# Kernel optimization log

Hardware: AMD Instinct MI355X
Metric: run time of the kernel (lower is better)

The kernel has to match this reference:

```python
import jax, jax.numpy as jnp
import numpy as np

D = 256       # dim
M = 50        # num_celltypes
NPATH = 65536 # path tokens (256*256)
N = M + NPATH
FF = 3        # focusing_factor
K = 5         # dwc kernel size


def find_closest_factors(num):
    for i in range(int(num ** 0.5), 0, -1):
        if num % i == 0:
            return (i, num // i)
    return (1, num)


def setup_inputs() -> dict:
    key = jax.random.key(0)
    ks = jax.random.split(key, 16)
    def w(k, shape, s=0.02):
        return jax.random.normal(k, shape, dtype=jnp.float32) * s
    z = lambda *s: jnp.zeros(s, jnp.float32)
    return {
        "x": jax.random.normal(ks[0], (1, N, D), dtype=jnp.float32),
        "W_qkv": w(ks[1], (D, 3 * D)),
        "scale_linear": w(ks[2], (1, 1, D)),
        "dwc_w": w(ks[3], (D, 1, K, K)),
        "dwc_b": w(ks[4], (D,)),
        "Wa": w(ks[5], (D, D)), "ba": z(D),
        "Wb": w(ks[6], (D, D)), "bb": z(D),
        "Wc": w(ks[7], (D, 1)), "bc": z(1),
        "W1": w(ks[8], (D, D)), "b1": z(D),
        "W2": w(ks[9], (D, D)), "b2": z(D),
        "W3a": w(ks[10], (2 * D, D)), "b3a": z(D),
        "W3b": w(ks[11], (D, D)), "b3b": z(D),
        "Wf": w(ks[12], (D, D)), "bf": z(D),
    }


def reference(x, W_qkv, scale_linear, dwc_w, dwc_b, Wa, ba, Wb, bb, Wc, bc,
              W1, b1, W2, b2, W3a, b3a, W3b, b3b, Wf, bf):
    scale = D ** -0.5
    qkv = x @ W_qkv                         # (1, N, 3D)
    q, k, v = jnp.split(qkv, 3, axis=-1)
    qc, qp = q[:, :M], q[:, M:]
    kc, kp = k[:, :M], k[:, M:]
    vc, vp = v[:, :M], v[:, M:]

    # --- softmax attention branches ---
    sa = jax.nn.softmax(jnp.einsum('bic,bjc->bij', qc * scale, kc), axis=-1)
    out_self_celltypes = sa @ vc            # (1, M, D)
    cap = jax.nn.softmax(jnp.einsum('bic,bjc->bij', qp * scale, kc), axis=-1)
    out_cross_path = cap @ vc               # (1, NPATH, D)
    cac = jax.nn.softmax(jnp.einsum('bic,bjc->bij', qc * scale, kp), axis=-1)
    out_cross_celltypes = cac @ vp          # (1, M, D)

    # --- focused linear attention on path tokens ---
    sp = jax.nn.softplus(scale_linear)
    ql = (jax.nn.relu(qp) + 1e-6) / sp
    kl = (jax.nn.relu(kp) + 1e-6) / sp
    qn = jnp.linalg.norm(ql, axis=-1, keepdims=True)
    kn = jnp.linalg.norm(kl, axis=-1, keepdims=True)
    ql = ql ** FF
    kl = kl ** FF
    ql = ql / jnp.linalg.norm(ql, axis=-1, keepdims=True) * qn
    kl = kl / jnp.linalg.norm(kl, axis=-1, keepdims=True) * kn
    zfac = 1.0 / (jnp.einsum('bic,bc->bi', ql, kl.sum(axis=1)) + 1e-6)
    kv = jnp.einsum('bjc,bjd->bcd', kl, vp)                 # (1, D, D)
    out_s = jnp.einsum('bic,bcd,bi->bid', ql, kv, zfac)     # (1, NPATH, D)

    # --- depthwise conv feature map ---
    wc, hc = find_closest_factors(NPATH)
    fm = vp.reshape(1, wc, hc, D).transpose(0, 3, 1, 2)     # b c w h
    fm = jax.lax.conv_general_dilated(
        fm, dwc_w, (1, 1), 'SAME',
        dimension_numbers=('NCHW', 'OIHW', 'NCHW'), feature_group_count=D)
    fm = fm + dwc_b[None, :, None, None]
    fm = fm.transpose(0, 2, 3, 1).reshape(1, NPATH, D)
    out_self_path = (out_s + fm) @ Wf + bf  # feamap_linear (dropout=eval)

    # --- gated attention net (shared weights, 4 calls) ---
    def gated(t):
        t = t[0]  # squeeze batch -> (n, D)
        a = jnp.tanh(t @ Wa + ba)
        g = jax.nn.sigmoid(t @ Wb + bb)
        return (a * g) @ Wc + bc  # (n, 1)

    A_cc = gated(out_cross_celltypes)
    A_cp = gated(out_cross_path)
    A_sc = gated(out_self_celltypes)
    A_sp = gated(out_self_path)

    # --- attention fusion (shared weights, 2 calls) ---
    def fuse(A1, A2, x1, x2):
        h1 = jax.nn.softmax(A1.T, axis=1) @ x1[0]   # (1, D)
        h1 = jax.nn.relu(h1 @ W1 + b1)
        h2 = jax.nn.softmax(A2.T, axis=1) @ x2[0]
        h2 = jax.nn.relu(h2 @ W2 + b2)
        f = jnp.concatenate([h1, h2], axis=1)       # (1, 2D)
        return jax.nn.relu(jax.nn.relu(f @ W3a + b3a) @ W3b + b3b)

    fusion_cross = fuse(A_cc, A_cp, out_cross_celltypes, out_cross_path)
    fusion_self = fuse(A_sc, A_sp, out_self_celltypes, out_self_path)
    return jnp.concatenate([fusion_cross, fusion_self], axis=1)  # (1, 2D)
```

## Files before the change

### kernel.cpp

```cpp
#include <hip/hip_runtime.h>
#include <hip/hip_bf16.h>
#include <math.h>


constexpr int DD = 256;
constexpr int MM = 50;
constexpr float SCL = 0.0625f;

constexpr size_t B_VPH = 0;
constexpr size_t B_QLH = (size_t)32 << 20;
constexpr size_t B_KLH = (size_t)64 << 20;
constexpr size_t B_E   = (size_t)96 << 20;
constexpr size_t B_SM  = (size_t)112 << 20;
constexpr size_t B_X   = B_SM + ((size_t)2 << 20);

constexpr size_t PP_OFF = (size_t)4 << 20;

constexpr size_t KLSUMR = 0;
constexpr size_t KLSUMP = 256;
constexpr size_t OCCDENP= 2304;
constexpr size_t W50P   = 2816;
constexpr size_t EDENP  = 3328;
constexpr size_t H2TP   = 3336;
constexpr size_t H2DENP = 5384;
constexpr size_t OCCRAW = 5392;
constexpr size_t ZEND   = 18192;
constexpr size_t QC     = ZEND;
constexpr size_t KC     = QC + 12800;
constexpr size_t VC     = KC + 12800;
constexpr size_t VCA    = VC + 12800;
constexpr size_t VCB    = VCA + 12800;
constexpr size_t WFA    = VCB + 12800;
constexpr size_t WFB    = WFA + 65536;
constexpr size_t BFA    = WFB + 65536;
constexpr size_t BFB    = BFA + 256;
constexpr size_t OSCB   = BFB + 256;
constexpr size_t OCCB   = OSCB + 12800;
constexpr size_t ASC    = OCCB + 12800;
constexpr size_t ACC50  = ASC + 64;
constexpr size_t SMEND  = ACC50 + 64;

constexpr size_t XT_WQKV = 0;
constexpr size_t XT_WFAT = 196608;
constexpr size_t XT_WFBT = 262144;
constexpr size_t XT_KVT  = 327680;
constexpr size_t XT_QCH  = 393216;
constexpr size_t XT_KCH  = 409600;
constexpr size_t XT_VCAT = 425984;
constexpr size_t XT_VCBT = 442368;
constexpr size_t XT_END  = 458752;
constexpr size_t WS_NEEDED = B_X + XT_END * 2;

typedef short bf16x8 __attribute__((ext_vector_type(8)));
typedef float f32x4 __attribute__((ext_vector_type(4)));

__device__ __forceinline__ float rcpf_(float x){ return __builtin_amdgcn_rcpf(x); }
__device__ __forceinline__ float fsig_(float x){ return rcpf_(1.0f + __expf(-x)); }
__device__ __forceinline__ float ftanh_(float x){ return 1.0f - 2.0f * rcpf_(__expf(2.0f * x) + 1.0f); }

__device__ __forceinline__ float bf2f(unsigned short u){
  return __uint_as_float(((unsigned int)u) << 16);
}
__device__ __forceinline__ unsigned short f2bf(float f){
  union { __hip_bfloat16 h; unsigned short u; } c;
  c.h = __float2bfloat16(f);
  return c.u;
}
__device__ __forceinline__ f32x4 mfma16(bf16x8 a, bf16x8 b, f32x4 c){
  return __builtin_amdgcn_mfma_f32_16x16x32_bf16(a, b, c, 0, 0, 0);
}

__device__ __forceinline__ float waveAllSum(float v){
  #pragma unroll
  for (int m = 1; m < 64; m <<= 1) v += __shfl_xor(v, m, 64);
  return v;
}

__device__ __forceinline__ size_t fragIdx(int n, int k, int K8){
  const int tile = n >> 4, cn = n & 15;
  const int k0 = k >> 5, kqi = (k >> 3) & 3, e = k & 7;
  return (((size_t)tile * K8 + k0) * 64 + (kqi * 16 + cn)) * 8 + e;
}

__device__ __forceinline__ int kvOff(int c, int k){
  return c * 40 + (c >> 3) * 8 + k;
}

__global__ void __launch_bounds__(256) k_prep0(const float* __restrict__ x, const float* __restrict__ Wqkv,
                                               float* qc, float* kc, float* vc,
                                               unsigned short* qch, unsigned short* kch,
                                               unsigned short* __restrict__ WT,
                                               const float* __restrict__ Wa, const float* __restrict__ Wb,
                                               const float* __restrict__ ba, const float* __restrict__ bb,
                                               const float* __restrict__ Wf, const float* __restrict__ bf,
                                               float* Wfa, float* Wfb, float* bfa, float* bfb,
                                               unsigned short* WfaTh, unsigned short* WfbTh){
  const int b = blockIdx.x, t = threadIdx.x;
  if (b < 48) {
    __shared__ unsigned short Tt[64][72];
    const int bn = b % 12, bk = b / 12;
    const int n0 = bn * 64, k0g = bk * 64;
    #pragma unroll
    for (int i = 0; i < 16; i++) {
      const int k_l = (t >> 6) + i * 4;
      const int n_l = t & 63;
      Tt[n_l][k_l] = f2bf(Wqkv[(size_t)(k0g + k_l) * 768 + n0 + n_l]);
    }
    __syncthreads();
    #pragma unroll
    for (int i = 0; i < 2; i++) {
      const int fr = t * 2 + i;
      const int t_l = fr >> 7;
      const int k0_l = (fr >> 6) & 1;
      const int lane_f = fr & 63;
      const int n_l = t_l * 16 + (lane_f & 15);
      const int k_l = k0_l * 32 + (lane_f >> 4) * 8;
      const int tg = (n0 >> 4) + t_l;
      const int k0gl = (k0g >> 5) + k0_l;
      bf16x8 v = *(const bf16x8*)&Tt[n_l][k_l];
      *(bf16x8*)&WT[(((size_t)tg * 8 + k0gl) * 64 + lane_f) * 8] = v;
    }
    return;
  }
  __shared__ float xs[256];
  const int j = t;
  if (b < 98) {
    const int r = b - 48;
    xs[j] = x[r * DD + j];
    __syncthreads();
    float aq = 0.f, ak = 0.f, av = 0.f;
    for (int k = 0; k < DD; k++) {
      float xv = xs[k];
      aq += xv * Wqkv[k * 768 + j];
      ak += xv * Wqkv[k * 768 + 256 + j];
      av += xv * Wqkv[k * 768 + 512 + j];
    }
    qc[r * DD + j] = aq; kc[r * DD + j] = ak; vc[r * DD + j] = av;
    qch[fragIdx(r, j, 8)] = f2bf(aq);
    kch[fragIdx(r, j, 8)] = f2bf(ak);
    if (r == 0) {
      for (int c = 50; c < 64; c++) {
        qch[fragIdx(c, j, 8)] = 0;
        kch[fragIdx(c, j, 8)] = 0;
      }
    }
    return;
  }
  const int bb2 = b - 98;
  const float* src; const float* Wm;
  if (bb2 < 256)      { src = Wf + bb2 * DD;         Wm = Wa; }
  else if (bb2 < 512) { src = Wf + (bb2 - 256) * DD; Wm = Wb; }
  else if (bb2 == 512){ src = bf;                    Wm = Wa; }
  else                { src = bf;                    Wm = Wb; }
  xs[j] = src[j];
  __syncthreads();
  float a = 0.f;
  for (int k = 0; k < DD; k++) a += xs[k] * Wm[k * DD + j];
  if (bb2 < 256)      { Wfa[bb2 * DD + j] = a; WfaTh[fragIdx(j, bb2, 8)] = f2bf(a); }
  else if (bb2 < 512) { Wfb[(bb2 - 256) * DD + j] = a; WfbTh[fragIdx(j, bb2 - 256, 8)] = f2bf(a); }
  else if (bb2 == 512) bfa[j] = a + ba[j];
  else bfb[j] = a + bb[j];
}

__global__ void __launch_bounds__(256) k_prep1g(const float* __restrict__ vc,
                                                const float* __restrict__ qc, const float* __restrict__ kc,
                                                const float* __restrict__ Wa, const float* __restrict__ Wb,
                                                const float* __restrict__ ba, const float* __restrict__ bb,
                                                const float* __restrict__ Wc, const float* __restrict__ bc,
                                                float* Vca, float* Vcb,
                                                unsigned short* VcaTh, unsigned short* VcbTh,
                                                float* __restrict__ osc, float* __restrict__ A){
  const int b = blockIdx.x, t = threadIdx.x;
  if (b < 50) {
    __shared__ float rs[256];
    const int r = b, j = t;
    rs[j] = vc[r * DD + j];
    __syncthreads();
    float a = 0.f, bv = 0.f;
    for (int k = 0; k < DD; k++) { float v = rs[k]; a += v * Wa[k * DD + j]; bv += v * Wb[k * DD + j]; }
    Vca[r * DD + j] = a; Vcb[r * DD + j] = bv;
    VcaTh[fragIdx(j, r, 2)] = f2bf(a);
    VcbTh[fragIdx(j, r, 2)] = f2bf(bv);
    if (r == 0) {
      for (int c = 50; c < 64; c++) {
        VcaTh[fragIdx(j, c, 2)] = 0;
        VcbTh[fragIdx(j, c, 2)] = 0;
      }
    }
    return;
  }
  const int i = b - 50;
  __shared__ float qs[256];
  __shared__ float P[64];
  __shared__ float red[4];
  qs[t] = qc[i * DD + t];
  __syncthreads();
  if (t < 64) {
    float s = -1e30f;
    if (t < 50) {
      float acc = 0.f;
      const float4* kr = (const float4*)&kc[t * DD];
      #pragma unroll 8
      for (int k = 0; k < 64; k++) {
        float4 kv = kr[k];
        float4 qv = *(const float4*)&qs[k * 4];
        acc += qv.x * kv.x + qv.y * kv.y + qv.z * kv.z + qv.w * kv.w;
      }
      s = acc * SCL;
    }
    float mx = s;
    #pragma unroll
    for (int m = 1; m < 64; m <<= 1) mx = fmaxf(mx, __shfl_xor(mx, m, 64));
    float e = (t < 50) ? __expf(s - mx) : 0.f;
    float den = waveAllSum(e);
    P[t] = e * rcpf_(den);
  }
  __syncthreads();
  float a = 0.f;
  for (int jj = 0; jj < 50; jj++) a += P[jj] * vc[jj * DD + t];
  osc[i * DD + t] = a;
  __syncthreads();
  qs[t] = a;
  __syncthreads();
  float u = 0.f, v = 0.f;
  for (int k = 0; k < DD; k++) { float tv = qs[k]; u += tv * Wa[k * DD + t]; v += tv * Wb[k * DD + t]; }
  float g = ftanh_(u + ba[t]) * fsig_(v + bb[t]) * Wc[t];
  g = waveAllSum(g);
  const int lane = t & 63, wv = t >> 6;
  if (lane == 0) red[wv] = g;
  __syncthreads();
  if (t == 0) A[i] = red[0] + red[1] + red[2] + red[3] + bc[0];
}

__global__ void __launch_bounds__(256) k_path1(
    const float* __restrict__ x, const unsigned short* __restrict__ WTf,
    const float* __restrict__ sln,
    const unsigned short* __restrict__ kchf, const unsigned short* __restrict__ qchf,
    const unsigned short* __restrict__ VcaTf, const unsigned short* __restrict__ VcbTf,
    const float* __restrict__ ba, const float* __restrict__ bb,
    const float* __restrict__ Wc, const float* __restrict__ bc,
    unsigned short* __restrict__ vph, unsigned short* __restrict__ qlh, unsigned short* __restrict__ klh,
    unsigned short* __restrict__ Eh, float* __restrict__ w50p, float* __restrict__ edenp, float* __restrict__ occdenp){
  __shared__ __align__(16) char arena[38912];
  unsigned short (*Psh)[72]   = (unsigned short (*)[72])arena;
  float (*denp)[4]            = (float (*)[4])(arena + 4608);
  unsigned short (*qpsb)[264] = (unsigned short (*)[264])(arena + 5120);
  unsigned short (*kpsb)[264] = (unsigned short (*)[264])(arena + 22016);

  const int tid = threadIdx.x;
  const int i0 = blockIdx.x * 32;
  const int part = blockIdx.x & 7;
  const int lane = tid & 63;
  const int wvv = tid >> 6;
  const int cn = lane & 15;
  const int m0 = (lane >> 4) * 4;
  const int kq = (lane >> 4) * 8;

  for (int l = tid; l < 2048; l += 256) {
    const int r = l >> 6, c4 = (l & 63) * 4;
    const float4 xv = *(const float4*)&x[(size_t)(MM + i0 + r) * DD + c4];
    ushort4 o; o.x = f2bf(xv.x); o.y = f2bf(xv.y); o.z = f2bf(xv.z); o.w = f2bf(xv.w);
    *(ushort4*)&qpsb[r][c4] = o;
  }
  __syncthreads();

  bf16x8 af0[8], af1[8];
  #pragma unroll
  for (int k0 = 0; k0 < 8; k0++) {
    af0[k0] = *(const bf16x8*)&qpsb[cn][k0 * 32 + kq];
    af1[k0] = *(const bf16x8*)&qpsb[16 + cn][k0 * 32 + kq];
  }
  __syncthreads();

  bf16x8 b0[8], b1[8];
  {
    const unsigned short* Bt = WTf + ((size_t)wvv * 8 * 64 + lane) * 8;
    #pragma unroll
    for (int k0 = 0; k0 < 8; k0++) b0[k0] = *(const bf16x8*)&Bt[(size_t)k0 * 512];
  }
  #pragma unroll 1
  for (int tt = 0; tt < 12; tt++) {
    const int t = wvv + 4 * tt;
    if (tt + 1 < 12) {
      const unsigned short* Bt = WTf + (((size_t)(t + 4) * 8) * 64 + lane) * 8;
      #pragma unroll
      for (int k0 = 0; k0 < 8; k0++) b1[k0] = *(const bf16x8*)&Bt[(size_t)k0 * 512];
    }
    f32x4 acc0 = {0.f, 0.f, 0.f, 0.f};
    f32x4 acc1 = {0.f, 0.f, 0.f, 0.f};
    #pragma unroll
    for (int k0 = 0; k0 < 8; k0++) {
      acc0 = mfma16(af0[k0], b0[k0], acc0);
      acc1 = mfma16(af1[k0], b0[k0], acc1);
    }
    if (t < 16) {
      int c = t * 16 + cn;
      #pragma unroll
      for (int i = 0; i < 4; i++) {
        qpsb[m0 + i][c] = f2bf(acc0[i]);
        qpsb[16 + m0 + i][c] = f2bf(acc1[i]);
      }
    } else if (t < 32) {
      int c = (t - 16) * 16 + cn;
      #pragma unroll
      for (int i = 0; i < 4; i++) {
        kpsb[m0 + i][c] = f2bf(acc0[i]);
        kpsb[16 + m0 + i][c] = f2bf(acc1[i]);
      }
    } else {
      int c = (t - 32) * 16 + cn;
      #pragma unroll
      for (int i = 0; i < 4; i++) {
        vph[(size_t)(i0 + m0 + i) * DD + c] = f2bf(acc0[i]);
        vph[(size_t)(i0 + 16 + m0 + i) * DD + c] = f2bf(acc1[i]);
      }
    }
    #pragma unroll
    for (int k0 = 0; k0 < 8; k0++) b0[k0] = b1[k0];
  }
  __syncthreads();

  float ep0[4], ep1[4];
  {
    f32x4 accp0 = {0.f,0.f,0.f,0.f}, accp1 = {0.f,0.f,0.f,0.f};
    f32x4 accc0 = {0.f,0.f,0.f,0.f}, accc1 = {0.f,0.f,0.f,0.f};
    const unsigned short* Bk = kchf + ((size_t)wvv * 8 * 64 + lane) * 8;
    const unsigned short* Bq = qchf + ((size_t)wvv * 8 * 64 + lane) * 8;
    #pragma unroll
    for (int k0 = 0; k0 < 8; k0++) {
      bf16x8 aq0 = *(const bf16x8*)&qpsb[cn][k0 * 32 + kq];
      bf16x8 aq1 = *(const bf16x8*)&qpsb[16 + cn][k0 * 32 + kq];
      bf16x8 ak0 = *(const bf16x8*)&kpsb[cn][k0 * 32 + kq];
      bf16x8 ak1 = *(const bf16x8*)&kpsb[16 + cn][k0 * 32 + kq];
      bf16x8 bk = *(const bf16x8*)&Bk[(size_t)k0 * 512];
      bf16x8 bq = *(const bf16x8*)&Bq[(size_t)k0 * 512];
      accp0 = mfma16(aq0, bk, accp0);
      accp1 = mfma16(aq1, bk, accp1);
      accc0 = mfma16(ak0, bq, accc0);
      accc1 = mfma16(ak1, bq, accc1);
    }
    const int col = wvv * 16 + cn;
    const bool ok = (col < 50);
    #pragma unroll
    for (int i = 0; i < 4; i++) {
      ep0[i] = ok ? __expf(accp0[i] * SCL) : 0.f;
      ep1[i] = ok ? __expf(accp1[i] * SCL) : 0.f;
    }
    float osum = 0.f;
    #pragma unroll
    for (int i = 0; i < 4; i++) {
      unsigned short h0 = ok ? f2bf(__expf(accc0[i] * SCL)) : (unsigned short)0;
      unsigned short h1 = ok ? f2bf(__expf(accc1[i] * SCL)) : (unsigned short)0;
      Eh[(size_t)(i0 + m0 + i) * 64 + col] = h0;
      Eh[(size_t)(i0 + 16 + m0 + i) * 64 + col] = h1;
      if (ok) osum += bf2f(h0) + bf2f(h1);
    }
    osum += __shfl_xor(osum, 16, 64);
    osum += __shfl_xor(osum, 32, 64);
    if (lane < 16 && ok) atomicAdd(&occdenp[part * 64 + col], osum);
    float d0[4], d1[4];
    #pragma unroll
    for (int i = 0; i < 4; i++) { d0[i] = ep0[i]; d1[i] = ep1[i]; }
    #pragma unroll
    for (int m = 1; m < 16; m <<= 1) {
      #pragma unroll
      for (int i = 0; i < 4; i++) {
        d0[i] += __shfl_xor(d0[i], m, 64);
        d1[i] += __shfl_xor(d1[i], m, 64);
      }
    }
    if (cn == 0) {
      #pragma unroll
      for (int i = 0; i < 4; i++) {
        denp[m0 + i][wvv] = d0[i];
        denp[16 + m0 + i][wvv] = d1[i];
      }
    }
  }
  __syncthreads();

  {
    const int col = wvv * 16 + cn;
    #pragma unroll
    for (int i = 0; i < 4; i++) {
      float4 dp = *(const float4*)&denp[m0 + i][0];
      Psh[m0 + i][col] = f2bf(ep0[i] * rcpf_(dp.x + dp.y + dp.z + dp.w));
      float4 dq = *(const float4*)&denp[16 + m0 + i][0];
      Psh[16 + m0 + i][col] = f2bf(ep1[i] * rcpf_(dq.x + dq.y + dq.z + dq.w));
    }
  }

  float4 sl4 = ((const float4*)sln)[lane];
  float4 rsp;
  rsp.x = rcpf_(log1pf(expf(sl4.x))); rsp.y = rcpf_(log1pf(expf(sl4.y)));
  rsp.z = rcpf_(log1pf(expf(sl4.z))); rsp.w = rcpf_(log1pf(expf(sl4.w)));
  float4 ba4 = ((const float4*)ba)[lane];
  float4 bb4 = ((const float4*)bb)[lane];
  float4 wc4 = ((const float4*)Wc)[lane];
  float bcv = bc[0];
  for (int rr = 0; rr < 8; rr++) {
    const int r = wvv * 8 + rr;
    const int row = i0 + r;
    ushort4 qu = *(const ushort4*)&qpsb[r][lane * 4];
    ushort4 ku = *(const ushort4*)&kpsb[r][lane * 4];
    float4 q4 = {bf2f(qu.x), bf2f(qu.y), bf2f(qu.z), bf2f(qu.w)};
    float4 k4 = {bf2f(ku.x), bf2f(ku.y), bf2f(ku.z), bf2f(ku.w)};
    float4 lq, lk;
    lq.x = (fmaxf(q4.x, 0.f) + 1e-6f) * rsp.x; lq.y = (fmaxf(q4.y, 0.f) + 1e-6f) * rsp.y;
    lq.z = (fmaxf(q4.z, 0.f) + 1e-6f) * rsp.z; lq.w = (fmaxf(q4.w, 0.f) + 1e-6f) * rsp.w;
    lk.x = (fmaxf(k4.x, 0.f) + 1e-6f) * rsp.x; lk.y = (fmaxf(k4.y, 0.f) + 1e-6f) * rsp.y;
    lk.z = (fmaxf(k4.z, 0.f) + 1e-6f) * rsp.z; lk.w = (fmaxf(k4.w, 0.f) + 1e-6f) * rsp.w;
    float4 q3, k3;
    q3.x = lq.x*lq.x*lq.x; q3.y = lq.y*lq.y*lq.y; q3.z = lq.z*lq.z*lq.z; q3.w = lq.w*lq.w*lq.w;
    k3.x = lk.x*lk.x*lk.x; k3.y = lk.y*lk.y*lk.y; k3.z = lk.z*lk.z*lk.z; k3.w = lk.w*lk.w*lk.w;
    float n1q = lq.x*lq.x + lq.y*lq.y + lq.z*lq.z + lq.w*lq.w;
    float n3q = q3.x*q3.x + q3.y*q3.y + q3.z*q3.z + q3.w*q3.w;
    float n1k = lk.x*lk.x + lk.y*lk.y + lk.z*lk.z + lk.w*lk.w;
    float n3k = k3.x*k3.x + k3.y*k3.y + k3.z*k3.z + k3.w*k3.w;
    n1q = waveAllSum(n1q); n3q = waveAllSum(n3q);
    n1k = waveAllSum(n1k); n3k = waveAllSum(n3k);
    float fq = sqrtf(n1q * rcpf_(n3q));
    float fk = sqrtf(n1k * rcpf_(n3k));
    ushort4 qo, ko;
    qo.x = f2bf(q3.x * fq); qo.y = f2bf(q3.y * fq); qo.z = f2bf(q3.z * fq); qo.w = f2bf(q3.w * fq);
    ko.x = f2bf(k3.x * fk); ko.y = f2bf(k3.y * fk); ko.z = f2bf(k3.z * fk); ko.w = f2bf(k3.w * fk);
    *(ushort4*)&qlh[(size_t)row * DD + lane * 4] = qo;
    *(ushort4*)&klh[(size_t)row * DD + lane * 4] = ko;
  }
  __syncthreads();

  {
    bf16x8 ap0[2], ap1[2];
    #pragma unroll
    for (int k0 = 0; k0 < 2; k0++) {
      ap0[k0] = *(const bf16x8*)&Psh[cn][k0 * 32 + kq];
      ap1[k0] = *(const bf16x8*)&Psh[16 + cn][k0 * 32 + kq];
    }
    #pragma unroll 1
    for (int tt = 0; tt < 4; tt++) {
      const int nt = wvv * 4 + tt;
      const unsigned short* Bu = VcaTf + (((size_t)nt * 2) * 64 + lane) * 8;
      const unsigned short* Bv = VcbTf + (((size_t)nt * 2) * 64 + lane) * 8;
      f32x4 au0 = {0.f,0.f,0.f,0.f}, au1 = {0.f,0.f,0.f,0.f};
      f32x4 av0 = {0.f,0.f,0.f,0.f}, av1 = {0.f,0.f,0.f,0.f};
      #pragma unroll
      for (int k0 = 0; k0 < 2; k0++) {
        bf16x8 bu = *(const bf16x8*)&Bu[(size_t)k0 * 512];
        bf16x8 bv = *(const bf16x8*)&Bv[(size_t)k0 * 512];
        au0 = mfma16(ap0[k0], bu, au0);
        au1 = mfma16(ap1[k0], bu, au1);
        av0 = mfma16(ap0[k0], bv, av0);
        av1 = mfma16(ap1[k0], bv, av1);
      }
      #pragma unroll
      for (int i = 0; i < 4; i++) {
        qpsb[m0 + i][nt * 16 + cn] = f2bf(au0[i]);
        qpsb[16 + m0 + i][nt * 16 + cn] = f2bf(au1[i]);
        kpsb[m0 + i][nt * 16 + cn] = f2bf(av0[i]);
        kpsb[16 + m0 + i][nt * 16 + cn] = f2bf(av1[i]);
      }
    }
  }
  __syncthreads();

  #pragma unroll
  for (int rr = 0; rr < 8; rr++) {
    const int r = wvv * 8 + rr;
    ushort4 uu = *(const ushort4*)&qpsb[r][lane * 4];
    ushort4 vv = *(const ushort4*)&kpsb[r][lane * 4];
    float g = ftanh_(bf2f(uu.x) + ba4.x) * fsig_(bf2f(vv.x) + bb4.x) * wc4.x
            + ftanh_(bf2f(uu.y) + ba4.y) * fsig_(bf2f(vv.y) + bb4.y) * wc4.y
            + ftanh_(bf2f(uu.z) + ba4.z) * fsig_(bf2f(vv.z) + bb4.z) * wc4.z
            + ftanh_(bf2f(uu.w) + ba4.w) * fsig_(bf2f(vv.w) + bb4.w) * wc4.w;
    g = waveAllSum(g);
    if (lane == 0) *(float*)&Psh[r][64] = __expf(g + bcv);
  }
  __syncthreads();
  if (tid < 64) {
    float s = 0.f;
    #pragma unroll
    for (int r = 0; r < 32; r++) s += *(const float*)&Psh[r][64] * bf2f(Psh[r][tid]);
    atomicAdd(&w50p[part * 64 + tid], s);
  }
  if (tid == 0) {
    float es = 0.f;
    #pragma unroll
    for (int r = 0; r < 32; r++) es += *(const float*)&Psh[r][64];
    atomicAdd(&edenp[part], es);
  }
}

__global__ void __launch_bounds__(256) k_kv(const unsigned short* __restrict__ klh,
                                            const unsigned short* __restrict__ Eh,
                                            const unsigned short* __restrict__ vph,
                                            unsigned short* __restrict__ PP,
                                            float* __restrict__ klsump,
                                            float* __restrict__ occraw){
  __shared__ __align__(16) unsigned short AT[2][2608];
  __shared__ __align__(16) unsigned short BvpT[2][10480];
  const int tid = threadIdx.x;
  const int lane = tid & 63;
  const int wvv = tid >> 6;
  const int cn = lane & 15;
  const int m0 = (lane >> 4) * 4;
  const int kq = (lane >> 4) * 8;
  const int cb = blockIdx.x;
  const int z  = blockIdx.y;
  const int jj = tid >> 3;
  const int c8 = (tid & 7) * 8;
  const bool isOcc = (cb == 4);

  f32x4 acc[4][4];
  f32x4 acc1[4];
  #pragma unroll
  for (int mt = 0; mt < 4; mt++) {
    acc1[mt] = (f32x4){0.f,0.f,0.f,0.f};
    #pragma unroll
    for (int tl = 0; tl < 4; tl++) acc[mt][tl] = (f32x4){0.f,0.f,0.f,0.f};
  }
  bf16x8 ones;
  #pragma unroll
  for (int i = 0; i < 8; i++) ones[i] = (short)0x3F80;

  const int jbase = z * 1024;
  {
    const int j0 = jbase;
    bf16x8 av;
    if (isOcc) av = *(const bf16x8*)&Eh[(size_t)(j0 + jj) * 64 + c8];
    else       av = *(const bf16x8*)&klh[(size_t)(j0 + jj) * 256 + cb * 64 + c8];
    #pragma unroll
    for (int i = 0; i < 8; i++) AT[0][kvOff(c8 + i, jj)] = (unsigned short)av[i];
    #pragma unroll
    for (int rep = 0; rep < 4; rep++) {
      bf16x8 bv = *(const bf16x8*)&vph[(size_t)(j0 + jj) * 256 + rep * 64 + c8];
      #pragma unroll
      for (int i = 0; i < 8; i++) BvpT[0][kvOff(rep * 64 + c8 + i, jj)] = (unsigned short)bv[i];
    }
  }
  __syncthreads();

  #pragma unroll 1
  for (int step = 0; step < 32; step++) {
    const int cur = step & 1;
    bf16x8 avn, bvn[4];
    if (step + 1 < 32) {
      const int j0 = jbase + (step + 1) * 32;
      if (isOcc) avn = *(const bf16x8*)&Eh[(size_t)(j0 + jj) * 64 + c8];
      else       avn = *(const bf16x8*)&klh[(size_t)(j0 + jj) * 256 + cb * 64 + c8];
      #pragma unroll
      for (int rep = 0; rep < 4; rep++)
        bvn[rep] = *(const bf16x8*)&vph[(size_t)(j0 + jj) * 256 + rep * 64 + c8];
    }
    bf16x8 afr[4], bfr[4];
    #pragma unroll
    for (int mt = 0; mt < 4; mt++)
      afr[mt] = *(const bf16x8*)&AT[cur][kvOff(cn + mt * 16, kq)];
    #pragma unroll
    for (int tl = 0; tl < 4; tl++)
      bfr[tl] = *(const bf16x8*)&BvpT[cur][kvOff(wvv * 64 + tl * 16 + cn, kq)];
    if (!isOcc) {
      #pragma unroll
      for (int mt = 0; mt < 4; mt++) acc1[mt] = mfma16(afr[mt], ones, acc1[mt]);
    }
    #pragma unroll
    for (int mt = 0; mt < 4; mt++)
      #pragma unroll
      for (int tl = 0; tl < 4; tl++) acc[mt][tl] = mfma16(afr[mt], bfr[tl], acc[mt][tl]);
    if (step + 1 < 32) {
      const int nb = cur ^ 1;
      #pragma unroll
      for (int i = 0; i < 8; i++) AT[nb][kvOff(c8 + i, jj)] = (unsigned short)avn[i];
      #pragma unroll
      for (int rep = 0; rep < 4; rep++)
        #pragma unroll
        for (int i = 0; i < 8; i++) BvpT[nb][kvOff(rep * 64 + c8 + i, jj)] = (unsigned short)bvn[rep][i];
    }
    __syncthreads();
  }
  if (isOcc) {
    #pragma unroll
    for (int mt = 0; mt < 4; mt++)
      #pragma unroll
      for (int i = 0; i < 4; i++) {
        const int ri = mt * 16 + m0 + i;
        if (ri < 50) {
          #pragma unroll
          for (int tl = 0; tl < 4; tl++) {
            const int d = wvv * 64 + tl * 16 + cn;
            atomicAdd(&occraw[ri * DD + d], acc[mt][tl][i]);
          }
        }
      }
    return;
  }
  unsigned short* P = PP + ((size_t)(cb * 64 + z)) * 16384;
  #pragma unroll
  for (int mt = 0; mt < 4; mt++)
    #pragma unroll
    for (int tl = 0; tl < 4; tl++) {
      const int n = (wvv * 4 + tl) * 16 + cn;
      #pragma unroll
      for (int i = 0; i < 4; i++)
        P[(size_t)(mt * 16 + m0 + i) * 256 + n] = f2bf(acc[mt][tl][i]);
    }
  if (wvv == 0 && cn == 0) {
    #pragma unroll
    for (int mt = 0; mt < 4; mt++)
      #pragma unroll
      for (int i = 0; i < 4; i++)
        atomicAdd(&klsump[(z & 7) * 256 + cb * 64 + mt * 16 + m0 + i], acc1[mt][i]);
  }
}

__global__ void __launch_bounds__(256) k_fin2(const unsigned short* __restrict__ PP,
                                              unsigned short* __restrict__ kvTf,
                                              const float* __restrict__ occraw,
                                              const float* __restrict__ occdenp,
                                              float* __restrict__ occ,
                                              const float* __restrict__ klsump,
                                              float* __restrict__ klsum,
                                              const float* __restrict__ Wa, const float* __restrict__ Wb,
                                              const float* __restrict__ ba, const float* __restrict__ bb,
                                              const float* __restrict__ Wc, const float* __restrict__ bc,
                                              float* __restrict__ A){
  __shared__ float ts[256];
  __shared__ float red[4];
  const int b = blockIdx.x, tid = threadIdx.x;
  if (b < 32) {
    const int gm = b * 8 + (tid >> 5);
    const int cb = gm >> 6, m = gm & 63;
    const int d8 = (tid & 31) * 8;
    float s[8];
    #pragma unroll
    for (int e = 0; e < 8; e++) s[e] = 0.f;
    for (int z = 0; z < 64; z++) {
      bf16x8 v = *(const bf16x8*)&PP[((size_t)(cb * 64 + z)) * 16384 + (size_t)m * 256 + d8];
      #pragma unroll
      for (int e = 0; e < 8; e++) s[e] += bf2f((unsigned short)v[e]);
    }
    #pragma unroll
    for (int e = 0; e < 8; e++)
      kvTf[fragIdx(d8 + e, gm, 8)] = f2bf(s[e]);
  } else if (b < 82) {
    const int i = b - 32, j = tid;
    float den = 0.f;
    #pragma unroll
    for (int p = 0; p < 8; p++) den += occdenp[p * 64 + i];
    float t = occraw[i * DD + j] / den;
    occ[i * DD + j] = t;
    ts[j] = t;
    __syncthreads();
    float u = 0.f, v = 0.f;
    for (int k = 0; k < DD; k++) { float tv = ts[k]; u += tv * Wa[k * DD + j]; v += tv * Wb[k * DD + j]; }
    float g = ftanh_(u + ba[j]) * fsig_(v + bb[j]) * Wc[j];
    g = waveAllSum(g);
    const int lane = j & 63, wv = j >> 6;
    if (lane == 0) red[wv] = g;
    __syncthreads();
    if (j == 0) A[i] = red[0] + red[1] + red[2] + red[3] + bc[0];
  } else {
    const int d = tid;
    float s = 0.f;
    #pragma unroll
    for (int p = 0; p < 8; p++) s += klsump[p * 256 + d];
    klsum[d] = s;
  }
}

__global__ void __launch_bounds__(256) k_tail(const unsigned short* __restrict__ qlh,
                                              const unsigned short* __restrict__ kvTf,
                                              const float* __restrict__ klsum,
                                              const unsigned short* __restrict__ vph,
                                              const float* __restrict__ dwcw, const float* __restrict__ dwcb,
                                              const unsigned short* __restrict__ WfaTf,
                                              const unsigned short* __restrict__ WfbTf,
                                              const float* __restrict__ bfa, const float* __restrict__ bfb,
                                              const float* __restrict__ Wc, const float* __restrict__ bc,
                                              float* __restrict__ h2tp, float* __restrict__ h2denp){
  __shared__ unsigned short Tsh[32][264];
  __shared__ unsigned short OSb[32][264];
  __shared__ unsigned short aVb[32][264];
  __shared__ float zf[32];
  __shared__ float ev[32];
  const int tid = threadIdx.x;
  const int i0 = blockIdx.x * 32;
  const int part = blockIdx.x & 7;
  const int lane = tid & 63;
  const int wvv = tid >> 6;
  const int cn = lane & 15;
  const int m0 = (lane >> 4) * 4;
  const int kq = (lane >> 4) * 8;
  for (int l = tid; l < 2048; l += 256) {
    int r = l >> 6, c4 = (l & 63) * 4;
    *(ushort4*)&Tsh[r][c4] = *(const ushort4*)&qlh[(size_t)(i0 + r) * DD + c4];
  }
  __syncthreads();
  {
    bf16x8 afq0[8], afq1[8];
    #pragma unroll
    for (int k0 = 0; k0 < 8; k0++) {
      afq0[k0] = *(const bf16x8*)&Tsh[cn][k0 * 32 + kq];
      afq1[k0] = *(const bf16x8*)&Tsh[16 + cn][k0 * 32 + kq];
    }
    #pragma unroll 1
    for (int tt = 0; tt < 4; tt++) {
      const int nt = wvv * 4 + tt;
      const unsigned short* Bt = kvTf + (((size_t)nt * 8) * 64 + lane) * 8;
      f32x4 acc0 = {0.f,0.f,0.f,0.f};
      f32x4 acc1 = {0.f,0.f,0.f,0.f};
      #pragma unroll
      for (int k0 = 0; k0 < 8; k0++) {
        bf16x8 b = *(const bf16x8*)&Bt[(size_t)k0 * 512];
        acc0 = mfma16(afq0[k0], b, acc0);
        acc1 = mfma16(afq1[k0], b, acc1);
      }
      #pragma unroll
      for (int i = 0; i < 4; i++) {
        OSb[m0 + i][nt * 16 + cn] = f2bf(acc0[i]);
        OSb[16 + m0 + i][nt * 16 + cn] = f2bf(acc1[i]);
      }
    }
  }
  {
    float4 ks4 = ((const float4*)klsum)[lane];
    #pragma unroll
    for (int rr = 0; rr < 8; rr++) {
      const int r = wvv * 8 + rr;
      ushort4 q4 = *(const ushort4*)&Tsh[r][lane * 4];
      float s = bf2f(q4.x)*ks4.x + bf2f(q4.y)*ks4.y + bf2f(q4.z)*ks4.z + bf2f(q4.w)*ks4.w;
      s = waveAllSum(s);
      if (lane == 0) zf[r] = rcpf_(s + 1e-6f);
    }
  }
  __syncthreads();
  const int j = tid;
  float w[25];
  #pragma unroll
  for (int t = 0; t < 25; t++) w[t] = dwcw[j * 25 + t];
  const float bias = dwcb[j];
  const int y = i0 >> 8, x0 = i0 & 255;
  float fm[32];
  #pragma unroll
  for (int r = 0; r < 32; r++) fm[r] = bias;
  #pragma unroll
  for (int dy = -2; dy <= 2; dy++) {
    const int yy = y + dy;
    if ((unsigned)yy > 255u) continue;
    float buf[36];
    #pragma unroll
    for (int i = 0; i < 36; i++) {
      const int xx = x0 - 2 + i;
      buf[i] = ((unsigned)xx <= 255u) ? bf2f(vph[(size_t)((yy << 8) + xx) * DD + j]) : 0.f;
    }
    const float* wr = &w[(dy + 2) * 5];
    #pragma unroll
    for (int r = 0; r < 32; r++)
      fm[r] += buf[r] * wr[0] + buf[r+1] * wr[1] + buf[r+2] * wr[2]
             + buf[r+3] * wr[3] + buf[r+4] * wr[4];
  }
  #pragma unroll
  for (int r = 0; r < 32; r++) {
    fm[r] = bf2f(OSb[r][j]) * zf[r] + fm[r];
    Tsh[r][j] = f2bf(fm[r]);
  }
  __syncthreads();
  {
    bf16x8 aft0[8], aft1[8];
    #pragma unroll
    for (int k0 = 0; k0 < 8; k0++) {
      aft0[k0] = *(const bf16x8*)&Tsh[cn][k0 * 32 + kq];
      aft1[k0] = *(const bf16x8*)&Tsh[16 + cn][k0 * 32 + kq];
    }
    #pragma unroll 1
    for (int jb = 0; jb < 8; jb++) {
      const int nt = wvv * 4 + (jb & 3);
      const unsigned short* Bt = ((jb < 4) ? WfaTf : WfbTf) + (((size_t)nt * 8) * 64 + lane) * 8;
      f32x4 acc0 = {0.f,0.f,0.f,0.f};
      f32x4 acc1 = {0.f,0.f,0.f,0.f};
      #pragma unroll
      for (int k0 = 0; k0 < 8; k0++) {
        bf16x8 b = *(const bf16x8*)&Bt[(size_t)k0 * 512];
        acc0 = mfma16(aft0[k0], b, acc0);
        acc1 = mfma16(aft1[k0], b, acc1);
      }
      unsigned short (*dst)[264] = (jb < 4) ? OSb : aVb;
      #pragma unroll
      for (int i = 0; i < 4; i++) {
        dst[m0 + i][nt * 16 + cn] = f2bf(acc0[i]);
        dst[16 + m0 + i][nt * 16 + cn] = f2bf(acc1[i]);
      }
    }
  }
  __syncthreads();
  {
    float4 bfa4 = ((const float4*)bfa)[lane];
    float4 bfb4 = ((const float4*)bfb)[lane];
    float4 wc4 = ((const float4*)Wc)[lane];
    const float bcv = bc[0];
    #pragma unroll
    for (int rr = 0; rr < 8; rr++) {
      const int r = wvv * 8 + rr;
      ushort4 uu = *(const ushort4*)&OSb[r][lane * 4];
      ushort4 vv = *(const ushort4*)&aVb[r][lane * 4];
      float g = ftanh_(bf2f(uu.x) + bfa4.x) * fsig_(bf2f(vv.x) + bfb4.x) * wc4.x
              + ftanh_(bf2f(uu.y) + bfa4.y) * fsig_(bf2f(vv.y) + bfb4.y) * wc4.y
              + ftanh_(bf2f(uu.z) + bfa4.z) * fsig_(bf2f(vv.z) + bfb4.z) * wc4.z
              + ftanh_(bf2f(uu.w) + bfa4.w) * fsig_(bf2f(vv.w) + bfb4.w) * wc4.w;
      g = waveAllSum(g);
      if (lane == 0) ev[r] = __expf(g + bcv);
    }
  }
  __syncthreads();
  float hp = 0.f;
  #pragma unroll
  for (int r = 0; r < 32; r++) hp += ev[r] * fm[r];
  atomicAdd(&h2tp[part * 256 + j], hp);
  if (tid == 0) {
    float es = 0.f;
    #pragma unroll
    for (int r = 0; r < 32; r++) es += ev[r];
    atomicAdd(&h2denp[part], es);
  }
}

__global__ void __launch_bounds__(256) k_final(
    const float* __restrict__ A_cc, const float* __restrict__ occ,
    const float* __restrict__ A_sc, const float* __restrict__ osc,
    const float* __restrict__ w50p, const float* __restrict__ edenp,
    const float* __restrict__ h2tp, const float* __restrict__ h2denp,
    const float* __restrict__ vc, const float* __restrict__ Wf, const float* __restrict__ bf,
    const float* __restrict__ W1, const float* __restrict__ b1,
    const float* __restrict__ W2, const float* __restrict__ b2,
    const float* __restrict__ W3a, const float* __restrict__ b3a,
    const float* __restrict__ W3b, const float* __restrict__ b3b,
    float* __restrict__ out){
  int j = threadIdx.x;
  __shared__ float pw[64];
  __shared__ float w50t[64];
  __shared__ float t1[256], t2[256], fz[512], z1[256];
  if (blockIdx.x == 0) {
    if (j < 64) {
      float s = 0.f;
      #pragma unroll
      for (int p = 0; p < 8; p++) s += w50p[p * 64 + j];
      w50t[j] = s;
    }
    float edentot = 0.f;
    #pragma unroll
    for (int p = 0; p < 8; p++) edentot += edenp[p];
    if (j < 64) pw[j] = (j < 50) ? expf(A_cc[j]) : 0.f;
    __syncthreads();
    float den = 0.f;
    for (int i = 0; i < 50; i++) den += pw[i];
    float raw = 0.f;
    for (int i = 0; i < 50; i++) raw += pw[i] * occ[i * DD + j];
    t1[j] = raw / den;
    float r2 = 0.f;
    for (int i = 0; i < 50; i++) r2 += w50t[i] * vc[i * DD + j];
    t2[j] = r2 / edentot;
    __syncthreads();
    float a1 = 0.f, a2 = 0.f;
    for (int k = 0; k < DD; k++) { a1 += t1[k] * W1[k * DD + j]; a2 += t2[k] * W2[k * DD + j]; }
    fz[j] = fmaxf(a1 + b1[j], 0.f);
    fz[256 + j] = fmaxf(a2 + b2[j], 0.f);
    __syncthreads();
    float z = 0.f;
    for (int k = 0; k < 512; k++) z += fz[k] * W3a[k * DD + j];
    z1[j] = fmaxf(z + b3a[j], 0.f);
    __syncthreads();
    float o = 0.f;
    for (int k = 0; k < DD; k++) o += z1[k] * W3b[k * DD + j];
    out[j] = fmaxf(o + b3b[j], 0.f);
  } else {
    float h2dentot = 0.f;
    #pragma unroll
    for (int p = 0; p < 8; p++) h2dentot += h2denp[p];
    if (j < 64) pw[j] = (j < 50) ? expf(A_sc[j]) : 0.f;
    {
      float s = 0.f;
      #pragma unroll
      for (int p = 0; p < 8; p++) s += h2tp[p * 256 + j];
      t2[j] = s / h2dentot;
    }
    __syncthreads();
    float den = 0.f;
    for (int i = 0; i < 50; i++) den += pw[i];
    float raw = 0.f;
    for (int i = 0; i < 50; i++) raw += pw[i] * osc[i * DD + j];
    t1[j] = raw / den;
    float hs = 0.f;
    for (int k = 0; k < DD; k++) hs += t2[k] * Wf[k * DD + j];
    __syncthreads();
    t2[j] = hs + bf[j];
    __syncthreads();
    float a1 = 0.f, a2 = 0.f;
    for (int k = 0; k < DD; k++) { a1 += t1[k] * W1[k * DD + j]; a2 += t2[k] * W2[k * DD + j]; }
    fz[j] = fmaxf(a1 + b1[j], 0.f);
    fz[256 + j] = fmaxf(a2 + b2[j], 0.f);
    __syncthreads();
    float z = 0.f;
    for (int k = 0; k < 512; k++) z += fz[k] * W3a[k * DD + j];
    z1[j] = fmaxf(z + b3a[j], 0.f);
    __syncthreads();
    float o = 0.f;
    for (int k = 0; k < DD; k++) o += z1[k] * W3b[k * DD + j];
    out[256 + j] = fmaxf(o + b3b[j], 0.f);
  }
}

extern "C" void kernel_launch(void* const* d_in, const int* in_sizes, int n_in,
                              void* d_out, int out_size, void* d_ws, size_t ws_size,
                              hipStream_t stream) {
  if (ws_size < WS_NEEDED) return;
  const float* x   = (const float*)d_in[0];
  const float* Wqkv= (const float*)d_in[1];
  const float* sln = (const float*)d_in[2];
  const float* dwcw= (const float*)d_in[3];
  const float* dwcb= (const float*)d_in[4];
  const float* Wa  = (const float*)d_in[5];
  const float* ba  = (const float*)d_in[6];
  const float* Wb  = (const float*)d_in[7];
  const float* bb  = (const float*)d_in[8];
  const float* Wc  = (const float*)d_in[9];
  const float* bc  = (const float*)d_in[10];
  const float* W1  = (const float*)d_in[11];
  const float* b1  = (const float*)d_in[12];
  const float* W2  = (const float*)d_in[13];
  const float* b2  = (const float*)d_in[14];
  const float* W3a = (const float*)d_in[15];
  const float* b3a = (const float*)d_in[16];
  const float* W3b = (const float*)d_in[17];
  const float* b3b = (const float*)d_in[18];
  const float* Wf  = (const float*)d_in[19];
  const float* bf  = (const float*)d_in[20];

  char* wsb = (char*)d_ws;
  unsigned short* VPH = (unsigned short*)(wsb + B_VPH);
  unsigned short* QLH = (unsigned short*)(wsb + B_QLH);
  unsigned short* KLH = (unsigned short*)(wsb + B_KLH);
  unsigned short* EHB = (unsigned short*)(wsb + B_E);
  unsigned short* PPB = EHB + PP_OFF;
  float* SM = (float*)(wsb + B_SM);
  unsigned short* XT = (unsigned short*)(wsb + B_X);
  float* outp = (float*)d_out;

  hipMemsetAsync((void*)SM, 0, ZEND * sizeof(float), stream);

  k_prep0<<<612, 256, 0, stream>>>(x, Wqkv, SM + QC, SM + KC, SM + VC,
                                   XT + XT_QCH, XT + XT_KCH, XT + XT_WQKV,
                                   Wa, Wb, ba, bb, Wf, bf,
                                   SM + WFA, SM + WFB, SM + BFA, SM + BFB,
                                   XT + XT_WFAT, XT + XT_WFBT);
  k_prep1g<<<100, 256, 0, stream>>>(SM + VC, SM + QC, SM + KC,
                                    Wa, Wb, ba, bb, Wc, bc,
                                    SM + VCA, SM + VCB, XT + XT_VCAT, XT + XT_VCBT,
                                    SM + OSCB, SM + ASC);

  k_path1<<<2048, 256, 0, stream>>>(x, XT + XT_WQKV, sln, XT + XT_KCH, XT + XT_QCH,
                                    XT + XT_VCAT, XT + XT_VCBT, ba, bb, Wc, bc,
                                    VPH, QLH, KLH, EHB, SM + W50P, SM + EDENP, SM + OCCDENP);
  k_kv<<<dim3(5, 64), 256, 0, stream>>>(KLH, EHB, VPH, PPB, SM + KLSUMP, SM + OCCRAW);
  k_fin2<<<83, 256, 0, stream>>>(PPB, XT + XT_KVT,
                                 SM + OCCRAW, SM + OCCDENP, SM + OCCB,
                                 SM + KLSUMP, SM + KLSUMR,
                                 Wa, Wb, ba, bb, Wc, bc, SM + ACC50);

  k_tail<<<2048, 256, 0, stream>>>(QLH, XT + XT_KVT, SM + KLSUMR, VPH, dwcw, dwcb,
                                   XT + XT_WFAT, XT + XT_WFBT, SM + BFA, SM + BFB,
                                   Wc, bc, SM + H2TP, SM + H2DENP);

  k_final<<<2, 256, 0, stream>>>(SM + ACC50, SM + OCCB, SM + ASC, SM + OSCB,
                                 SM + W50P, SM + EDENP, SM + H2TP, SM + H2DENP,
                                 SM + VC, Wf, bf, W1, b1, W2, b2, W3a, b3a, W3b, b3b, outp);
}
```

Measured before the change: 470.1 us.

## Accumulate KV partials via fp32 atomics and double token split in k_kv

k_kv now adds each block's KV partial into a single fp32 accumulator with atomicAdd instead of writing per-slice bf16 partial buffers. k_fin2 then only converts that accumulator to the fragment layout, with no 64-way reduction. The token range per block is halved and the grid doubled to 5x128 for more parallelism. This removes the partial-buffer write and read-back, but adds many contended global atomics and changes the summation order.

New measurement: 500.2 us. 6.4% more time.

```diff
diff --git a/kernel.cpp b/kernel.cpp
--- a/kernel.cpp
+++ b/kernel.cpp
@@ -13,8 +13,6 @@
 constexpr size_t B_E   = (size_t)96 << 20;
 constexpr size_t B_SM  = (size_t)112 << 20;
 constexpr size_t B_X   = B_SM + ((size_t)2 << 20);
-
-constexpr size_t PP_OFF = (size_t)4 << 20;
 
 constexpr size_t KLSUMR = 0;
 constexpr size_t KLSUMP = 256;
@@ -24,7 +22,8 @@
 constexpr size_t H2TP   = 3336;
 constexpr size_t H2DENP = 5384;
 constexpr size_t OCCRAW = 5392;
-constexpr size_t ZEND   = 18192;
+constexpr size_t KVACC  = 18192;
+constexpr size_t ZEND   = KVACC + 65536;
 constexpr size_t QC     = ZEND;
 constexpr size_t KC     = QC + 12800;
 constexpr size_t VC     = KC + 12800;
@@ -493,7 +492,7 @@
 __global__ void __launch_bounds__(256) k_kv(const unsigned short* __restrict__ klh,
                                             const unsigned short* __restrict__ Eh,
                                             const unsigned short* __restrict__ vph,
-                                            unsigned short* __restrict__ PP,
+                                            float* __restrict__ kvacc,
                                             float* __restrict__ klsump,
                                             float* __restrict__ occraw){
   __shared__ __align__(16) unsigned short AT[2][2608];
@@ -522,7 +521,7 @@
   #pragma unroll
   for (int i = 0; i < 8; i++) ones[i] = (short)0x3F80;
 
-  const int jbase = z * 1024;
+  const int jbase = z * 512;
   {
     const int j0 = jbase;
     bf16x8 av;
@@ -540,10 +539,10 @@
   __syncthreads();
 
   #pragma unroll 1
-  for (int step = 0; step < 32; step++) {
+  for (int step = 0; step < 16; step++) {
     const int cur = step & 1;
     bf16x8 avn, bvn[4];
-    if (step + 1 < 32) {
+    if (step + 1 < 16) {
       const int j0 = jbase + (step + 1) * 32;
       if (isOcc) avn = *(const bf16x8*)&Eh[(size_t)(j0 + jj) * 64 + c8];
       else       avn = *(const bf16x8*)&klh[(size_t)(j0 + jj) * 256 + cb * 64 + c8];
@@ -566,7 +565,7 @@
     for (int mt = 0; mt < 4; mt++)
       #pragma unroll
       for (int tl = 0; tl < 4; tl++) acc[mt][tl] = mfma16(afr[mt], bfr[tl], acc[mt][tl]);
-    if (step + 1 < 32) {
+    if (step + 1 < 16) {
       const int nb = cur ^ 1;
       #pragma unroll
       for (int i = 0; i < 8; i++) AT[nb][kvOff(c8 + i, jj)] = (unsigned short)avn[i];
@@ -593,7 +592,6 @@
       }
     return;
   }
-  unsigned short* P = PP + ((size_t)(cb * 64 + z)) * 16384;
   #pragma unroll
   for (int mt = 0; mt < 4; mt++)
     #pragma unroll
@@ -601,7 +599,7 @@
       const int n = (wvv * 4 + tl) * 16 + cn;
       #pragma unroll
       for (int i = 0; i < 4; i++)
-        P[(size_t)(mt * 16 + m0 + i) * 256 + n] = f2bf(acc[mt][tl][i]);
+        atomicAdd(&kvacc[(size_t)(cb * 64 + mt * 16 + m0 + i) * 256 + n], acc[mt][tl][i]);
     }
   if (wvv == 0 && cn == 0) {
     #pragma unroll
@@ -612,7 +610,7 @@
   }
 }
 
-__global__ void __launch_bounds__(256) k_fin2(const unsigned short* __restrict__ PP,
+__global__ void __launch_bounds__(256) k_fin2(const float* __restrict__ kvacc,
                                               unsigned short* __restrict__ kvTf,
                                               const float* __restrict__ occraw,
                                               const float* __restrict__ occdenp,
@@ -626,23 +624,19 @@
   __shared__ float ts[256];
   __shared__ float red[4];
   const int b = blockIdx.x, tid = threadIdx.x;
-  if (b < 32) {
-    const int gm = b * 8 + (tid >> 5);
-    const int cb = gm >> 6, m = gm & 63;
-    const int d8 = (tid & 31) * 8;
-    float s[8];
-    #pragma unroll
-    for (int e = 0; e < 8; e++) s[e] = 0.f;
-    for (int z = 0; z < 64; z++) {
-      bf16x8 v = *(const bf16x8*)&PP[((size_t)(cb * 64 + z)) * 16384 + (size_t)m * 256 + d8];
-      #pragma unroll
-      for (int e = 0; e < 8; e++) s[e] += bf2f((unsigned short)v[e]);
-    }
-    #pragma unroll
-    for (int e = 0; e < 8; e++)
-      kvTf[fragIdx(d8 + e, gm, 8)] = f2bf(s[e]);
-  } else if (b < 82) {
-    const int i = b - 32, j = tid;
+  if (b < 8) {
+    const int gm = b * 32 + (tid >> 3);
+    const int d0 = (tid & 7) * 32;
+    #pragma unroll 8
+    for (int q = 0; q < 8; q++) {
+      float4 v = *(const float4*)&kvacc[(size_t)gm * 256 + d0 + q * 4];
+      kvTf[fragIdx(d0 + q * 4 + 0, gm, 8)] = f2bf(v.x);
+      kvTf[fragIdx(d0 + q * 4 + 1, gm, 8)] = f2bf(v.y);
+      kvTf[fragIdx(d0 + q * 4 + 2, gm, 8)] = f2bf(v.z);
+      kvTf[fragIdx(d0 + q * 4 + 3, gm, 8)] = f2bf(v.w);
+    }
+  } else if (b < 58) {
+    const int i = b - 8, j = tid;
     float den = 0.f;
     #pragma unroll
     for (int p = 0; p < 8; p++) den += occdenp[p * 64 + i];
@@ -939,7 +933,6 @@
   unsigned short* QLH = (unsigned short*)(wsb + B_QLH);
   unsigned short* KLH = (unsigned short*)(wsb + B_KLH);
   unsigned short* EHB = (unsigned short*)(wsb + B_E);
-  unsigned short* PPB = EHB + PP_OFF;
   float* SM = (float*)(wsb + B_SM);
   unsigned short* XT = (unsigned short*)(wsb + B_X);
   float* outp = (float*)d_out;
@@ -959,8 +952,8 @@
   k_path1<<<2048, 256, 0, stream>>>(x, XT + XT_WQKV, sln, XT + XT_KCH, XT + XT_QCH,
                                     XT + XT_VCAT, XT + XT_VCBT, ba, bb, Wc, bc,
                                     VPH, QLH, KLH, EHB, SM + W50P, SM + EDENP, SM + OCCDENP);
-  k_kv<<<dim3(5, 64), 256, 0, stream>>>(KLH, EHB, VPH, PPB, SM + KLSUMP, SM + OCCRAW);
-  k_fin2<<<83, 256, 0, stream>>>(PPB, XT + XT_KVT,
+  k_kv<<<dim3(5, 128), 256, 0, stream>>>(KLH, EHB, VPH, SM + KVACC, SM + KLSUMP, SM + OCCRAW);
+  k_fin2<<<59, 256, 0, stream>>>(SM + KVACC, XT + XT_KVT,
                                  SM + OCCRAW, SM + OCCDENP, SM + OCCB,
                                  SM + KLSUMP, SM + KLSUMR,
                                  Wa, Wb, ba, bb, Wc, bc, SM + ACC50);
```
